# Optimization experiments

Hardware: AMD Instinct MI355X
Metric: run time of the kernel (lower is better)

Reference implementation:

```python
import jax, jax.numpy as jnp
import numpy as np

TOPK = 7  # matches init kwarg topk and conv kernel depth


def setup_inputs() -> dict:
    key = jax.random.key(0)
    k1, k2, k3 = jax.random.split(key, 3)
    b, c, h, w = 2, 64, 96, 96
    x = jax.random.normal(k1, (b, c, h, w), dtype=jnp.float32)
    # Conv3d(c, c, (topk,1,1)) weight squeezed to [out_c, in_c, topk]
    W = jax.random.normal(k2, (c, c, TOPK), dtype=jnp.float32) * 0.05
    bias = jax.random.normal(k3, (c,), dtype=jnp.float32) * 0.05
    return {"x": x, "W": W, "bias": bias}


def reference(x, W, bias):
    b, c, h, w = x.shape
    k = W.shape[2]  # topk
    hw = h * w
    X_ = x.reshape(b, c, hw)
    # L2-normalize over channel dim (cosine features)
    X = X_ / jnp.sqrt(jnp.sum(X_ * X_, axis=1, keepdims=True))
    # full pairwise similarity [b, hw, hw] (cut=1 path in dividing())
    score = jnp.einsum('bcm,bcn->bmn', X, X)
    vals, idx = jax.lax.top_k(score, k)          # [b, hw, k]
    valsT = jnp.transpose(vals, (0, 2, 1))       # [b, k, hw]
    idxT = jnp.transpose(idx, (0, 2, 1))         # [b, k, hw]
    # gather unnormalized features of the top-k neighbors: [b, c, k, hw]
    gathered = jax.vmap(lambda Xb, ib: Xb[:, ib])(X_, idxT)
    high_d = gathered * valsT[:, None, :, :]     # weight by similarity score
    # Conv3d with kernel (k,1,1), no padding == contraction over (in_c, k)
    out = jnp.einsum('bikm,oik->bom', high_d, W) + bias[None, :, None]
    return jax.nn.relu(out).reshape(b, c, h, w)
```

## Files before the change

kernel.cpp:

```cpp
#include <hip/hip_runtime.h>
#include <math.h>

#define HW 9216
#define C 64
#define BATCH 2
#define K 7
#define NCH 16
#define CHUNK 576
#define NOUT 9
#define LTOP 8
#define NCAND 128
#define IK 448
#define GA_STRIDE 456

typedef __attribute__((ext_vector_type(8))) short bf16x8;
typedef __attribute__((ext_vector_type(16))) float f32x16;

#define GLOAD_LDS(gp, lp) __builtin_amdgcn_global_load_lds( \
    (const __attribute__((address_space(1))) unsigned int*)(gp), \
    (__attribute__((address_space(3))) unsigned int*)(lp), 16, 0, 0)

__device__ __forceinline__ unsigned umax_(unsigned a, unsigned b) {
#if defined(__has_builtin) && __has_builtin(__builtin_elementwise_max)
    return __builtin_elementwise_max(a, b);
#else
    return a >= b ? a : b;
#endif
}
__device__ __forceinline__ unsigned umin_(unsigned a, unsigned b) {
#if defined(__has_builtin) && __has_builtin(__builtin_elementwise_min)
    return __builtin_elementwise_min(a, b);
#else
    return a >= b ? b : a;
#endif
}

__device__ __forceinline__ unsigned short rne_bf16(float f) {
    unsigned u = __float_as_uint(f);
    unsigned r = u + 0x7fffu + ((u >> 16) & 1u);
    return (unsigned short)(r >> 16);
}

__device__ __forceinline__ void sort8_desc(unsigned (&k)[8]) {
#define CE8(i, j) { unsigned hi = umax_(k[i], k[j]); unsigned lo = umin_(k[i], k[j]); k[i] = hi; k[j] = lo; }
    CE8(0,1) CE8(2,3) CE8(4,5) CE8(6,7)
    CE8(0,2) CE8(1,3) CE8(4,6) CE8(5,7)
    CE8(1,2) CE8(5,6)
    CE8(0,4) CE8(1,5) CE8(2,6) CE8(3,7)
    CE8(2,4) CE8(3,5)
    CE8(1,2) CE8(3,4) CE8(5,6)
#undef CE8
}

__device__ __forceinline__ void merge8_desc(unsigned (&tv)[8], const unsigned (&s)[8]) {
    unsigned t[8];
#pragma unroll
    for (int i = 0; i < 8; ++i) t[i] = umax_(tv[i], s[7 - i]);
#define CET(i, j) { unsigned hi = umax_(t[i], t[j]); unsigned lo = umin_(t[i], t[j]); t[i] = hi; t[j] = lo; }
    CET(0,4) CET(1,5) CET(2,6) CET(3,7)
    CET(0,2) CET(1,3) CET(4,6) CET(5,7)
    CET(0,1) CET(2,3) CET(4,5) CET(6,7)
#undef CET
#pragma unroll
    for (int i = 0; i < 8; ++i) tv[i] = t[i];
}

__global__ __launch_bounds__(256) void k_norm(const float* __restrict__ x,
                                              const float* __restrict__ W,
                                              float* __restrict__ XT,
                                              unsigned short* __restrict__ Xhi,
                                              float* __restrict__ invn,
                                              unsigned short* __restrict__ WbT) {
    int b = blockIdx.y, tid = threadIdx.x;
    int bx = blockIdx.x;
    if (bx >= HW / 64) {
        if (b == 0) {
            int base = (bx - HW / 64) * 1024 + tid * 4;
#pragma unroll
            for (int j = 0; j < 4; ++j) {
                int idx = base + j;
                int o = idx / IK;
                int rem = idx - o * IK;
                int kq = rem >> 6, i = rem & 63;
                WbT[idx] = rne_bf16(W[(o * C + i) * K + kq]);
            }
        }
        return;
    }
    int m0 = bx * 64;
    __shared__ float T[64 * 65];
    __shared__ float ps[4][64];
    __shared__ float inv[64];
    const float* xb = x + (size_t)b * C * HW;
    for (int r = 0; r < 16; ++r) {
        int idx = r * 256 + tid; int c = idx >> 6, mm = idx & 63;
        T[c * 65 + mm] = xb[(size_t)c * HW + m0 + mm];
    }
    __syncthreads();
    int ml = tid & 63, part = tid >> 6;
    float s = 0.f;
    for (int c = part * 16; c < part * 16 + 16; ++c) { float v = T[c * 65 + ml]; s += v * v; }
    ps[part][ml] = s;
    __syncthreads();
    if (tid < 64) {
        float tot = ps[0][tid] + ps[1][tid] + ps[2][tid] + ps[3][tid];
        float iv = 1.0f / sqrtf(tot);
        inv[tid] = iv;
        invn[(size_t)b * HW + m0 + tid] = iv;
    }
    __syncthreads();
    for (int r = 0; r < 16; ++r) {
        int idx = r * 256 + tid; int row = idx >> 6, c = idx & 63;
        float uv = T[c * 65 + row];
        XT[((size_t)b * HW + m0 + row) * C + c] = uv;
        Xhi[((size_t)b * HW + m0 + row) * C + c] = rne_bf16(uv * inv[row]);
    }
}

__global__ __launch_bounds__(256) void k_score(const unsigned short* __restrict__ Xhi,
                                               unsigned* __restrict__ candi) {
    int mg = blockIdx.x, chunk = blockIdx.y, b = blockIdx.z;
    int tid = threadIdx.x;
    int w = tid >> 6, l = tid & 63;
    int lr = l & 31, lh = l >> 5;
    int m = mg * 128 + w * 32 + lr;
    const char* Xb = (const char*)(Xhi + (size_t)b * HW * C);

    __shared__ __align__(16) char tiles[2][8192];

    bf16x8 bf[4];
#pragma unroll
    for (int t = 0; t < 4; ++t)
        bf[t] = *(const bf16x8*)(Xb + (size_t)m * 128 + t * 32 + lh * 16);

    int swsrc = (tid * 16) ^ (((tid >> 3) & 7) << 4);
    int nC = chunk * CHUNK;

    GLOAD_LDS(Xb + (size_t)nC * 128 + swsrc, &tiles[0][w * 1024]);
    GLOAD_LDS(Xb + (size_t)nC * 128 + 4096 + swsrc, &tiles[0][4096 + w * 1024]);
    __syncthreads();

    unsigned tv[LTOP];
#pragma unroll
    for (int j = 0; j < LTOP; ++j) tv[j] = 0u;

    const float BIAS = 1.0625f;
    const f32x16 cbias = {BIAS,BIAS,BIAS,BIAS,BIAS,BIAS,BIAS,BIAS,
                          BIAS,BIAS,BIAS,BIAS,BIAS,BIAS,BIAS,BIAS};

    for (int so = 0; so < NOUT; ++so) {
        if (so + 1 < NOUT) {
            const char* src = Xb + (size_t)(nC + (so + 1) * 64) * 128;
            GLOAD_LDS(src + swsrc, &tiles[(so + 1) & 1][w * 1024]);
            GLOAD_LDS(src + 4096 + swsrc, &tiles[(so + 1) & 1][4096 + w * 1024]);
        }
        const char* tile = tiles[so & 1];
#pragma unroll
        for (int h = 0; h < 2; ++h) {
            bf16x8 af0 = *(const bf16x8*)(tile + (h * 32 + lr) * 128 + ((lh * 16) ^ ((lr & 7) << 4)));
            f32x16 acc = __builtin_amdgcn_mfma_f32_32x32x16_bf16(af0, bf[0], cbias, 0, 0, 0);
#pragma unroll
            for (int t = 1; t < 4; ++t) {
                int o = t * 32 + lh * 16;
                bf16x8 af = *(const bf16x8*)(tile + (h * 32 + lr) * 128 + (o ^ ((lr & 7) << 4)));
                acc = __builtin_amdgcn_mfma_f32_32x32x16_bf16(af, bf[t], acc, 0, 0, 0);
            }
            unsigned inv_base = 2047u - (unsigned)(so * 64 + h * 32 + 4 * lh);
            unsigned ka[8], kb[8];
#pragma unroll
            for (int r = 0; r < 8; ++r) {
                ka[r] = (__float_as_uint(acc[r]) & 0xFFFFF800u)
                      | (inv_base - (unsigned)((r & 3) + 8 * (r >> 2)));
                kb[r] = (__float_as_uint(acc[r + 8]) & 0xFFFFF800u)
                      | (inv_base - (unsigned)(((r + 8) & 3) + 8 * ((r + 8) >> 2)));
            }
            sort8_desc(ka);
            sort8_desc(kb);
            merge8_desc(tv, ka);
            merge8_desc(tv, kb);
        }
        __syncthreads();
    }

    unsigned pv[LTOP];
#pragma unroll
    for (int j = 0; j < LTOP; ++j) pv[j] = tv[j];
#pragma unroll
    for (int j = 0; j < LTOP; ++j) {
        unsigned o = (unsigned)__shfl_xor((int)pv[LTOP - 1 - j], 32, 64);
        tv[j] = umax_(tv[j], o);
    }
    if (lh == 0) {
        size_t base = ((size_t)(b * HW + m) * NCH + chunk) * LTOP;
#pragma unroll
        for (int j = 0; j < LTOP; ++j) candi[base + j] = tv[j];
    }
}

__global__ __launch_bounds__(256) void k_rescore(const float* __restrict__ XT,
                                                 const float* __restrict__ invn,
                                                 const unsigned* __restrict__ candi,
                                                 float* __restrict__ fvals,
                                                 int* __restrict__ fidx) {
    int g = blockIdx.x * 4 + (threadIdx.x >> 6);
    int l = threadIdx.x & 63;
    int b = g / HW, m = g - b * HW;
    const float* Xb = XT + (size_t)b * HW * C;
    float xml = Xb[(size_t)m * C + l];
    float vm = invn[g];

    unsigned k0 = candi[(size_t)g * NCAND + l];
    unsigned k1 = candi[(size_t)g * NCAND + 64 + l];

    unsigned thr = 0u;
#pragma unroll
    for (int bit = 30; bit >= 11; --bit) {
        unsigned cand = thr | (1u << bit);
        int cnt = __popcll(__ballot(k0 >= cand)) + __popcll(__ballot(k1 >= cand));
        if (cnt >= 7) thr = cand;
    }
    float s7 = __uint_as_float(thr);
    unsigned thk = __float_as_uint(s7 - 0.012f) & 0xFFFFF800u;

    unsigned long long bal0 = __ballot(k0 >= thk);
    unsigned long long bal1 = __ballot(k1 >= thk);

    float svv = -1e30f; int svi = 0x7fffffff;
    int nsurv = 0;
#pragma unroll
    for (int h = 0; h < 2; ++h) {
        unsigned long long bb = h ? bal1 : bal0;
        while (bb) {
            int src = __builtin_ctzll(bb);
            bb &= bb - 1;
            unsigned key = (unsigned)__shfl((int)(h ? k1 : k0), src, 64);
            int cpos = h * 64 + src;
            int ci = (cpos >> 3) * CHUNK + (2047 - (int)(key & 0x7FFu));
            float v = xml * Xb[(size_t)ci * C + l];
            v += __shfl_xor(v, 1, 64);  v += __shfl_xor(v, 2, 64);
            v += __shfl_xor(v, 4, 64);  v += __shfl_xor(v, 8, 64);
            v += __shfl_xor(v, 16, 64); v += __shfl_xor(v, 32, 64);
            if (l == nsurv) { svv = v * vm * invn[(size_t)b * HW + ci]; svi = ci; }
            ++nsurv;
        }
    }

    for (int s = 0; s < 7; ++s) {
        float bv = svv; int bi = svi;
#pragma unroll
        for (int d = 1; d < 64; d <<= 1) {
            float ov = __shfl_xor(bv, d, 64);
            int   oi = __shfl_xor(bi, d, 64);
            if (ov > bv || (ov == bv && oi < bi)) { bv = ov; bi = oi; }
        }
        if (l == 0) { fvals[(size_t)g * 7 + s] = bv; fidx[(size_t)g * 7 + s] = bi; }
        if (svi == bi) svv = -1e30f;
    }
}

__global__ __launch_bounds__(256) void k_out(const float* __restrict__ XT,
                                             const unsigned short* __restrict__ WbT,
                                             const float* __restrict__ fvals,
                                             const int* __restrict__ fidx,
                                             const float* __restrict__ bias,
                                             float* __restrict__ out) {
    int b = blockIdx.y;
    int m0 = blockIdx.x * 64;
    int tid = threadIdx.x;
    int w = tid >> 6, l = tid & 63;
    int lr = l & 31, hi = l >> 5;

    __shared__ __align__(16) unsigned short Ga[64][GA_STRIDE];
    __shared__ float Red[64][68];
    __shared__ int   fiL[64 * K];
    __shared__ float fvL[64 * K];

#pragma unroll
    for (int t = 0; t < 2; ++t) {
        int idx = t * 256 + tid;
        if (idx < 64 * K) {
            int gm = (b * HW + m0 + (idx / K)) * K + (idx % K);
            fiL[idx] = fidx[gm];
            fvL[idx] = fvals[gm];
        }
    }
    __syncthreads();

#pragma unroll
    for (int t = 0; t < 28; ++t) {
        int slot = t * 256 + tid;
        int r = slot >> 4, i4 = slot & 15;
        int m = r & 63, kq = r >> 6;
        int n = fiL[m * K + kq];
        float vv = fvL[m * K + kq];
        float4 g = *(const float4*)&XT[((size_t)b * HW + n) * C + i4 * 4];
        unsigned short h0 = rne_bf16(g.x * vv), h1 = rne_bf16(g.y * vv);
        unsigned short h2 = rne_bf16(g.z * vv), h3 = rne_bf16(g.w * vv);
        unsigned p0 = (unsigned)h0 | ((unsigned)h1 << 16);
        unsigned p1 = (unsigned)h2 | ((unsigned)h3 << 16);
        uint2 p = {p0, p1};
        *(uint2*)&Ga[m][kq * 64 + i4 * 4] = p;
    }
    __syncthreads();

    int mt = w & 1, ct = w >> 1;
    int arow = mt * 32 + lr;
    int ocol = ct * 32 + lr;
    float bv = bias[ocol];
    f32x16 acc;
#pragma unroll
    for (int r = 0; r < 16; ++r) acc[r] = bv;

    const unsigned short* wrow = WbT + (size_t)ocol * IK;
#pragma unroll
    for (int s = 0; s < 28; ++s) {
        bf16x8 af = *(const bf16x8*)&Ga[arow][s * 16 + hi * 8];
        bf16x8 bf = *(const bf16x8*)&wrow[s * 16 + hi * 8];
        acc = __builtin_amdgcn_mfma_f32_32x32x16_bf16(af, bf, acc, 0, 0, 0);
    }

#pragma unroll
    for (int j = 0; j < 4; ++j) {
        float4 r4 = {acc[j * 4 + 0], acc[j * 4 + 1], acc[j * 4 + 2], acc[j * 4 + 3]};
        *(float4*)&Red[ocol][mt * 32 + j * 8 + hi * 4] = r4;
    }
    __syncthreads();

#pragma unroll
    for (int t = 0; t < 4; ++t) {
        int slot4 = t * 256 + tid;
        int o = slot4 >> 4, m4 = slot4 & 15;
        float4 v = *(const float4*)&Red[o][m4 * 4];
        v.x = v.x > 0.f ? v.x : 0.f;
        v.y = v.y > 0.f ? v.y : 0.f;
        v.z = v.z > 0.f ? v.z : 0.f;
        v.w = v.w > 0.f ? v.w : 0.f;
        *(float4*)&out[((size_t)b * C + o) * HW + m0 + m4 * 4] = v;
    }
}

extern "C" void kernel_launch(void* const* d_in, const int* in_sizes, int n_in,
                              void* d_out, int out_size, void* d_ws, size_t ws_size,
                              hipStream_t stream) {
    const float* x = (const float*)d_in[0];
    const float* W = (const float*)d_in[1];
    const float* bias = (const float*)d_in[2];
    float* out = (float*)d_out;

    float* ws = (float*)d_ws;
    float* XT = ws;
    unsigned short* Xhi = (unsigned short*)(XT + (size_t)BATCH * HW * C);
    float* invn = (float*)(Xhi + (size_t)BATCH * HW * C);
    unsigned short* WbT = (unsigned short*)(invn + (size_t)BATCH * HW);
    unsigned* candi = (unsigned*)(WbT + (size_t)C * IK + 64);
    float* fvals = (float*)(candi + (size_t)BATCH * HW * NCAND);
    int* fidx = (int*)(fvals + (size_t)BATCH * HW * K);

    k_norm<<<dim3(HW / 64 + 28, BATCH), 256, 0, stream>>>(x, W, XT, Xhi, invn, WbT);
    k_score<<<dim3(HW / 128, NCH, BATCH), 256, 0, stream>>>(Xhi, candi);
    k_rescore<<<dim3(BATCH * HW / 4), 256, 0, stream>>>(XT, invn, candi, fvals, fidx);
    k_out<<<dim3(HW / 64, BATCH), 256, 0, stream>>>(XT, WbT, fvals, fidx, bias, out);
}
```

Measured before the change: 123.9 us.

## Split scoring into seed pass and threshold-filtered second pass with atomic candidate lists

Scoring becomes two passes. The first pass computes top-8 candidates over 4 of the 16 chunks. The second pass takes the merged 8th-best value minus a margin as a threshold, and over the other 12 chunks it appends only candidates above that threshold to a per-row list of up to 160 entries, using atomic counters. This replaces the per-chunk sort/merge network in most chunks with cheap compares, at the cost of atomics and scattered writes and an extra launch. Rescoring then reads the seed candidates plus the variable-length list, with a coarser key mask. There is a risk of truncation when the cap overflows.

Measured after the change: 203.2 us. 1.64x slower.

```diff
diff --git a/kernel.cpp b/kernel.cpp
--- a/kernel.cpp
+++ b/kernel.cpp
@@ -8,8 +8,8 @@
 #define NCH 16
 #define CHUNK 576
 #define NOUT 9
-#define LTOP 8
-#define NCAND 128
+#define P1CH 4
+#define CAP 160
 #define IK 448
 #define GA_STRIDE 456
 
@@ -52,15 +52,19 @@
 #undef CE8
 }
 
-__device__ __forceinline__ void merge8_desc(unsigned (&tv)[8], const unsigned (&s)[8]) {
-    unsigned t[8];
-#pragma unroll
-    for (int i = 0; i < 8; ++i) t[i] = umax_(tv[i], s[7 - i]);
+__device__ __forceinline__ void clean8_desc(unsigned (&t)[8]) {
 #define CET(i, j) { unsigned hi = umax_(t[i], t[j]); unsigned lo = umin_(t[i], t[j]); t[i] = hi; t[j] = lo; }
     CET(0,4) CET(1,5) CET(2,6) CET(3,7)
     CET(0,2) CET(1,3) CET(4,6) CET(5,7)
     CET(0,1) CET(2,3) CET(4,5) CET(6,7)
 #undef CET
+}
+
+__device__ __forceinline__ void merge8_desc(unsigned (&tv)[8], const unsigned (&s)[8]) {
+    unsigned t[8];
+#pragma unroll
+    for (int i = 0; i < 8; ++i) t[i] = umax_(tv[i], s[7 - i]);
+    clean8_desc(t);
 #pragma unroll
     for (int i = 0; i < 8; ++i) tv[i] = t[i];
 }
@@ -117,10 +121,12 @@
     }
 }
 
-__global__ __launch_bounds__(256) void k_score(const unsigned short* __restrict__ Xhi,
-                                               unsigned* __restrict__ candi) {
+__global__ __launch_bounds__(256) void k_score1(const unsigned short* __restrict__ Xhi,
+                                                unsigned* __restrict__ candi,
+                                                unsigned* __restrict__ cnt) {
     int mg = blockIdx.x, chunk = blockIdx.y, b = blockIdx.z;
     int tid = threadIdx.x;
+    if (chunk == 0 && tid < 128) cnt[b * HW + mg * 128 + tid] = 0u;
     int w = tid >> 6, l = tid & 63;
     int lr = l & 31, lh = l >> 5;
     int m = mg * 128 + w * 32 + lr;
@@ -140,9 +146,9 @@
     GLOAD_LDS(Xb + (size_t)nC * 128 + 4096 + swsrc, &tiles[0][4096 + w * 1024]);
     __syncthreads();
 
-    unsigned tv[LTOP];
-#pragma unroll
-    for (int j = 0; j < LTOP; ++j) tv[j] = 0u;
+    unsigned tv[8];
+#pragma unroll
+    for (int j = 0; j < 8; ++j) tv[j] = 0u;
 
     const float BIAS = 1.0625f;
     const f32x16 cbias = {BIAS,BIAS,BIAS,BIAS,BIAS,BIAS,BIAS,BIAS,
@@ -182,24 +188,107 @@
         __syncthreads();
     }
 
-    unsigned pv[LTOP];
-#pragma unroll
-    for (int j = 0; j < LTOP; ++j) pv[j] = tv[j];
-#pragma unroll
-    for (int j = 0; j < LTOP; ++j) {
-        unsigned o = (unsigned)__shfl_xor((int)pv[LTOP - 1 - j], 32, 64);
+    unsigned pv[8];
+#pragma unroll
+    for (int j = 0; j < 8; ++j) pv[j] = tv[j];
+#pragma unroll
+    for (int j = 0; j < 8; ++j) {
+        unsigned o = (unsigned)__shfl_xor((int)pv[7 - j], 32, 64);
         tv[j] = umax_(tv[j], o);
     }
+    clean8_desc(tv);
     if (lh == 0) {
-        size_t base = ((size_t)(b * HW + m) * NCH + chunk) * LTOP;
-#pragma unroll
-        for (int j = 0; j < LTOP; ++j) candi[base + j] = tv[j];
+        size_t base = ((size_t)(b * HW + m) * P1CH + chunk) * 8;
+#pragma unroll
+        for (int j = 0; j < 8; ++j) candi[base + j] = tv[j];
+    }
+}
+
+__global__ __launch_bounds__(256) void k_score2(const unsigned short* __restrict__ Xhi,
+                                                const unsigned* __restrict__ candi,
+                                                unsigned* __restrict__ cnt,
+                                                unsigned* __restrict__ glist) {
+    int mg = blockIdx.x, chunk = P1CH + blockIdx.y, b = blockIdx.z;
+    int tid = threadIdx.x;
+    int w = tid >> 6, l = tid & 63;
+    int lr = l & 31, lh = l >> 5;
+    int m = mg * 128 + w * 32 + lr;
+    int g = b * HW + m;
+    const char* Xb = (const char*)(Xhi + (size_t)b * HW * C);
+
+    const unsigned* p1 = candi + (size_t)g * (P1CH * 8);
+    unsigned t8[8], s8[8];
+#pragma unroll
+    for (int i = 0; i < 8; ++i) t8[i] = p1[i];
+#pragma unroll
+    for (int c = 1; c < P1CH; ++c) {
+#pragma unroll
+        for (int i = 0; i < 8; ++i) s8[i] = p1[c * 8 + i];
+        merge8_desc(t8, s8);
+    }
+    float tf = __uint_as_float(t8[7] & 0xFFFFF800u) - 0.010f;
+    unsigned thmb = __float_as_uint(tf);
+
+    __shared__ __align__(16) char tiles[2][8192];
+
+    bf16x8 bf[4];
+#pragma unroll
+    for (int t = 0; t < 4; ++t)
+        bf[t] = *(const bf16x8*)(Xb + (size_t)m * 128 + t * 32 + lh * 16);
+
+    int swsrc = (tid * 16) ^ (((tid >> 3) & 7) << 4);
+    int nC = chunk * CHUNK;
+
+    GLOAD_LDS(Xb + (size_t)nC * 128 + swsrc, &tiles[0][w * 1024]);
+    GLOAD_LDS(Xb + (size_t)nC * 128 + 4096 + swsrc, &tiles[0][4096 + w * 1024]);
+    __syncthreads();
+
+    const float BIAS = 1.0625f;
+    const f32x16 cbias = {BIAS,BIAS,BIAS,BIAS,BIAS,BIAS,BIAS,BIAS,
+                          BIAS,BIAS,BIAS,BIAS,BIAS,BIAS,BIAS,BIAS};
+
+    for (int so = 0; so < NOUT; ++so) {
+        if (so + 1 < NOUT) {
+            const char* src = Xb + (size_t)(nC + (so + 1) * 64) * 128;
+            GLOAD_LDS(src + swsrc, &tiles[(so + 1) & 1][w * 1024]);
+            GLOAD_LDS(src + 4096 + swsrc, &tiles[(so + 1) & 1][4096 + w * 1024]);
+        }
+        const char* tile = tiles[so & 1];
+#pragma unroll
+        for (int h = 0; h < 2; ++h) {
+            bf16x8 af0 = *(const bf16x8*)(tile + (h * 32 + lr) * 128 + ((lh * 16) ^ ((lr & 7) << 4)));
+            f32x16 acc = __builtin_amdgcn_mfma_f32_32x32x16_bf16(af0, bf[0], cbias, 0, 0, 0);
+#pragma unroll
+            for (int t = 1; t < 4; ++t) {
+                int o = t * 32 + lh * 16;
+                bf16x8 af = *(const bf16x8*)(tile + (h * 32 + lr) * 128 + (o ^ ((lr & 7) << 4)));
+                acc = __builtin_amdgcn_mfma_f32_32x32x16_bf16(af, bf[t], acc, 0, 0, 0);
+            }
+            int nbase = nC + so * 64 + h * 32 + 4 * lh;
+#pragma unroll
+            for (int r = 0; r < 16; ++r) {
+                unsigned hb = __float_as_uint(acc[r]);
+                bool hit = hb > thmb;
+                if (__any(hit)) {
+                    if (hit) {
+                        unsigned pos = atomicAdd(&cnt[g], 1u);
+                        if (pos < CAP) {
+                            unsigned nglob = (unsigned)(nbase + (r & 3) + 8 * (r >> 2));
+                            glist[(size_t)g * CAP + pos] = (hb & 0xFFFFC000u) | nglob;
+                        }
+                    }
+                }
+            }
+        }
+        __syncthreads();
     }
 }
 
 __global__ __launch_bounds__(256) void k_rescore(const float* __restrict__ XT,
                                                  const float* __restrict__ invn,
                                                  const unsigned* __restrict__ candi,
+                                                 const unsigned* __restrict__ cnt,
+                                                 const unsigned* __restrict__ glist,
                                                  float* __restrict__ fvals,
                                                  int* __restrict__ fidx) {
     int g = blockIdx.x * 4 + (threadIdx.x >> 6);
@@ -209,33 +298,45 @@
     float xml = Xb[(size_t)m * C + l];
     float vm = invn[g];
 
-    unsigned k0 = candi[(size_t)g * NCAND + l];
-    unsigned k1 = candi[(size_t)g * NCAND + 64 + l];
+    int cn = (int)cnt[g];
+    cn = cn < CAP ? cn : CAP;
+
+    unsigned kr[3];
+#pragma unroll
+    for (int h = 0; h < 3; ++h) {
+        int idx = h * 64 + l;
+        if (idx < P1CH * 8) {
+            unsigned key = candi[(size_t)g * (P1CH * 8) + idx];
+            unsigned n = (unsigned)((idx >> 3) * CHUNK + (2047 - (int)(key & 0x7FFu)));
+            kr[h] = (key & 0xFFFFC000u) | n;
+        } else {
+            int j = idx - P1CH * 8;
+            kr[h] = (j < cn) ? glist[(size_t)g * CAP + j] : 0u;
+        }
+    }
 
     unsigned thr = 0u;
 #pragma unroll
-    for (int bit = 30; bit >= 11; --bit) {
+    for (int bit = 30; bit >= 14; --bit) {
         unsigned cand = thr | (1u << bit);
-        int cnt = __popcll(__ballot(k0 >= cand)) + __popcll(__ballot(k1 >= cand));
-        if (cnt >= 7) thr = cand;
+        int c2 = __popcll(__ballot(kr[0] >= cand))
+               + __popcll(__ballot(kr[1] >= cand))
+               + __popcll(__ballot(kr[2] >= cand));
+        if (c2 >= 7) thr = cand;
     }
     float s7 = __uint_as_float(thr);
-    unsigned thk = __float_as_uint(s7 - 0.012f) & 0xFFFFF800u;
-
-    unsigned long long bal0 = __ballot(k0 >= thk);
-    unsigned long long bal1 = __ballot(k1 >= thk);
+    unsigned thk = __float_as_uint(s7 - 0.016f) & 0xFFFFC000u;
 
     float svv = -1e30f; int svi = 0x7fffffff;
     int nsurv = 0;
 #pragma unroll
-    for (int h = 0; h < 2; ++h) {
-        unsigned long long bb = h ? bal1 : bal0;
+    for (int h = 0; h < 3; ++h) {
+        unsigned long long bb = __ballot(kr[h] >= thk);
         while (bb) {
             int src = __builtin_ctzll(bb);
             bb &= bb - 1;
-            unsigned key = (unsigned)__shfl((int)(h ? k1 : k0), src, 64);
-            int cpos = h * 64 + src;
-            int ci = (cpos >> 3) * CHUNK + (2047 - (int)(key & 0x7FFu));
+            unsigned key = (unsigned)__shfl((int)kr[h], src, 64);
+            int ci = (int)(key & 0x3FFFu);
             float v = xml * Xb[(size_t)ci * C + l];
             v += __shfl_xor(v, 1, 64);  v += __shfl_xor(v, 2, 64);
             v += __shfl_xor(v, 4, 64);  v += __shfl_xor(v, 8, 64);
@@ -353,11 +454,14 @@
     float* invn = (float*)(Xhi + (size_t)BATCH * HW * C);
     unsigned short* WbT = (unsigned short*)(invn + (size_t)BATCH * HW);
     unsigned* candi = (unsigned*)(WbT + (size_t)C * IK + 64);
-    float* fvals = (float*)(candi + (size_t)BATCH * HW * NCAND);
+    unsigned* cnt = candi + (size_t)BATCH * HW * (P1CH * 8);
+    unsigned* glist = cnt + (size_t)BATCH * HW;
+    float* fvals = (float*)(glist + (size_t)BATCH * HW * CAP);
     int* fidx = (int*)(fvals + (size_t)BATCH * HW * K);
 
     k_norm<<<dim3(HW / 64 + 28, BATCH), 256, 0, stream>>>(x, W, XT, Xhi, invn, WbT);
-    k_score<<<dim3(HW / 128, NCH, BATCH), 256, 0, stream>>>(Xhi, candi);
-    k_rescore<<<dim3(BATCH * HW / 4), 256, 0, stream>>>(XT, invn, candi, fvals, fidx);
+    k_score1<<<dim3(HW / 128, P1CH, BATCH), 256, 0, stream>>>(Xhi, candi, cnt);
+    k_score2<<<dim3(HW / 128, NCH - P1CH, BATCH), 256, 0, stream>>>(Xhi, candi, cnt, glist);
+    k_rescore<<<dim3(BATCH * HW / 4), 256, 0, stream>>>(XT, invn, candi, cnt, glist, fvals, fidx);
     k_out<<<dim3(HW / 64, BATCH), 256, 0, stream>>>(XT, WbT, fvals, fidx, bias, out);
 }
```
